# Performance work log

Hardware: AMD Instinct MI355X
Metric: run time of the kernel (lower is better)

Reference implementation:

```python
import jax, jax.numpy as jnp
import numpy as np

VOCAB = 50000
OOV = 100
UNITS = 512
EMB = UNITS // 2
N_SENT = 32
N_WORDS = 50
B = 64


def setup_inputs() -> dict:
    key = jax.random.key(0)
    ks = jax.random.split(key, 16)
    g = lambda k, sh, s=0.02: (jax.random.normal(k, sh, dtype=jnp.float32) * s)
    inp = {
        "embedded_target": jax.random.normal(ks[0], (B, 1, EMB), dtype=jnp.float32),
        "hidden_dec": jax.random.normal(ks[1], (B, UNITS), dtype=jnp.float32),
        "encoded_sentences": jax.random.normal(ks[2], (B, N_SENT, UNITS), dtype=jnp.float32),
        "encoded_words": jax.random.normal(ks[3], (B, N_SENT, N_WORDS, UNITS), dtype=jnp.float32),
        "numeric_input": jax.random.randint(ks[4], (B, N_SENT * N_WORDS), 0, VOCAB + OOV),
        "batch_size": B,
        # GRU params (keras reset_after=True layout: 3 gates z,r,h stacked)
        "gru_Wx": g(ks[5], (EMB, 3 * UNITS)),
        "gru_Wh": g(ks[6], (UNITS, 3 * UNITS)),
        "gru_b": jnp.zeros((2, 3 * UNITS), dtype=jnp.float32),
        # attention params
        "W_att_sent": g(ks[7], (UNITS, UNITS)),
        "W_att_word": g(ks[8], (UNITS, UNITS)),
        # output projection (input is dec_units//2 after weight_dec)
        "fc_W": g(ks[9], (UNITS // 2, VOCAB)),
        "fc_b": jnp.zeros((VOCAB,), dtype=jnp.float32),
        "weight_context": g(ks[10], (UNITS, 1)),
        "weight_hidden": g(ks[11], (UNITS, 1)),
        "weight_dec": g(ks[12], (2 * UNITS, UNITS // 2)),
        "weight_input": g(ks[13], (UNITS // 2, 1)),
    }
    return inp


def _gru_step(x, h, Wx, Wh, b):
    # keras GRU cell, reset_after=True
    xm = x @ Wx + b[0]            # [B, 3U]
    hm = h @ Wh + b[1]            # [B, 3U]
    xz, xr, xh = jnp.split(xm, 3, axis=-1)
    hz, hr, hh = jnp.split(hm, 3, axis=-1)
    z = jax.nn.sigmoid(xz + hz)
    r = jax.nn.sigmoid(xr + hr)
    hcand = jnp.tanh(xh + r * hh)
    return z * h + (1.0 - z) * hcand


def reference(embedded_target, hidden_dec, encoded_sentences, encoded_words,
              gru_Wx, gru_Wh, gru_b, W_att_sent, W_att_word, fc_W, fc_b,
              weight_context, weight_hidden, weight_dec, weight_input,
              numeric_input, batch_size):
    # ---- GRU over the (length-1) target step; return last hidden ----
    def step(h, x_t):
        h2 = _gru_step(x_t, h, gru_Wx, gru_Wh, gru_b)
        return h2, None
    dec_output, _ = jax.lax.scan(step, hidden_dec, jnp.swapaxes(embedded_target, 0, 1))

    # ---- Luong (general) attention over sentences ----
    q = dec_output @ W_att_sent                              # [B, U]
    score_s = jnp.einsum("bd,bsd->bs", q, encoded_sentences)  # [B, S]
    alpha = jax.nn.softmax(score_s, axis=-1)                  # [B, S]
    context = jnp.einsum("bs,bsd->bd", alpha, encoded_sentences)  # [B, U]

    # ---- generation distribution ----
    x = jnp.concatenate([context, dec_output], axis=-1)       # [B, 2U]
    hidden_t = jnp.tanh(x @ weight_dec)                       # [B, U/2]
    gen_distr = jax.nn.softmax(hidden_t @ fc_W + fc_b, axis=-1)
    gen_distr = jnp.pad(gen_distr, ((0, 0), (0, OOV)))        # [B, V+OOV]

    # ---- hierarchical word attention (word softmax per sentence, scaled by alpha) ----
    qw = dec_output @ W_att_word                              # [B, U]
    score_w = jnp.einsum("bd,bswd->bsw", qw, encoded_words)   # [B, S, W]
    word_attn = jax.nn.softmax(score_w, axis=-1)              # softmax over words
    beta = (alpha[:, :, None] * word_attn).reshape(batch_size, -1)  # [B, S*W]

    # ---- batched scatter-add copy distribution ----
    ext = VOCAB + OOV
    bidx = jnp.arange(batch_size)[:, None]
    copy_distr = jnp.zeros((batch_size, ext), dtype=beta.dtype).at[bidx, numeric_input].add(beta)

    # ---- generation gate ----
    res1 = context @ weight_context
    res2 = dec_output @ weight_hidden
    res3 = embedded_target.reshape(batch_size, EMB) @ weight_input
    p_gen = jax.nn.sigmoid(res1 + res2 + res3)                # [B, 1]

    return dec_output, gen_distr, copy_distr, p_gen
```

## Files before the change

kernel.cpp:

```cpp
#include <hip/hip_runtime.h>

#define VOCAB 50000
#define OOV   100
#define EXT   50100
#define UNITS 512
#define EMB   256
#define NS    32
#define NW    50
#define BATCH 64
#define NQ    8
#define BINS_PER ((EXT + NQ - 1) / NQ)

#define GKC   24
#define QKC   8
#define HKC   16
#define CTXS  4
#define NCB   ((VOCAB + 63) / 64)

using short8 = __attribute__((ext_vector_type(8))) short;
using f32x4  = __attribute__((ext_vector_type(4))) float;

__device__ __forceinline__ float sigmoidf_(float x) { return 1.f / (1.f + __expf(-x)); }

__device__ __forceinline__ unsigned short f2bf(float x) {
  union { float f; unsigned u; } c; c.f = x;
  const unsigned r = (c.u + 0x7FFFu + ((c.u >> 16) & 1u)) >> 16;
  return (unsigned short)r;
}

__global__ __launch_bounds__(256) void k_gru_part(
    const float* __restrict__ emb, const float* __restrict__ h0,
    const float* __restrict__ Wx, const float* __restrict__ Wh,
    float* __restrict__ gates)
{
  __shared__ float sv[32];
  const int kc = blockIdx.x, b = blockIdx.y, t = threadIdx.x, u0 = 2 * t;
  const int base = kc * 32;
  const bool isx = base < EMB;
  if (t < 32) sv[t] = isx ? emb[b * EMB + base + t] : h0[b * UNITS + base - EMB + t];
  __syncthreads();

  const float* W = isx ? (Wx + (size_t)base * 1536) : (Wh + (size_t)(base - EMB) * 1536);
  float azx = 0.f, azy = 0.f, arx = 0.f, ary = 0.f, ahx = 0.f, ahy = 0.f;
  for (int i = 0; i < 32; i += 4) {
    float2 wz[4], wr[4], wh[4];
#pragma unroll
    for (int j = 0; j < 4; ++j) {
      const float* row = W + (size_t)(i + j) * 1536;
      wz[j] = *(const float2*)(row + u0);
      wr[j] = *(const float2*)(row + 512 + u0);
      wh[j] = *(const float2*)(row + 1024 + u0);
    }
#pragma unroll
    for (int j = 0; j < 4; ++j) {
      const float v = sv[i + j];
      azx = fmaf(v, wz[j].x, azx); azy = fmaf(v, wz[j].y, azy);
      arx = fmaf(v, wr[j].x, arx); ary = fmaf(v, wr[j].y, ary);
      ahx = fmaf(v, wh[j].x, ahx); ahy = fmaf(v, wh[j].y, ahy);
    }
  }
  float* gb_ = gates + (size_t)b * 2048;
  atomicAdd(gb_ + u0, azx);           atomicAdd(gb_ + u0 + 1, azy);
  atomicAdd(gb_ + 512 + u0, arx);     atomicAdd(gb_ + 512 + u0 + 1, ary);
  const int ho = isx ? 1024 : 1536;
  atomicAdd(gb_ + ho + u0, ahx);      atomicAdd(gb_ + ho + u0 + 1, ahy);
}

__global__ __launch_bounds__(256) void k_gru_fin(
    const float* __restrict__ gates, const float* __restrict__ gb,
    const float* __restrict__ h0, const float* __restrict__ emb,
    const float* __restrict__ whid, const float* __restrict__ winp,
    float* __restrict__ ws_dec, float* __restrict__ out_dec,
    float* __restrict__ ws_pgen)
{
  __shared__ float sred[256];
  const int b = blockIdx.x, t = threadIdx.x, u0 = 2 * t;
  const float* g_ = gates + (size_t)b * 2048;
  const float2 az  = *(const float2*)(g_ + u0);
  const float2 ar  = *(const float2*)(g_ + 512 + u0);
  const float2 ahx = *(const float2*)(g_ + 1024 + u0);
  const float2 ahh = *(const float2*)(g_ + 1536 + u0);

  const float2 b0z = *(const float2*)(gb + u0);
  const float2 b0r = *(const float2*)(gb + 512 + u0);
  const float2 b0h = *(const float2*)(gb + 1024 + u0);
  const float2 b1z = *(const float2*)(gb + 1536 + u0);
  const float2 b1r = *(const float2*)(gb + 1536 + 512 + u0);
  const float2 b1h = *(const float2*)(gb + 1536 + 1024 + u0);
  const float2 hp  = *(const float2*)(h0 + b * UNITS + u0);

  const float z0 = sigmoidf_(az.x + b0z.x + b1z.x);
  const float z1 = sigmoidf_(az.y + b0z.y + b1z.y);
  const float r0 = sigmoidf_(ar.x + b0r.x + b1r.x);
  const float r1 = sigmoidf_(ar.y + b0r.y + b1r.y);
  const float c0 = tanhf(ahx.x + b0h.x + r0 * (ahh.x + b1h.x));
  const float c1 = tanhf(ahx.y + b0h.y + r1 * (ahh.y + b1h.y));
  const float n0 = z0 * hp.x + (1.f - z0) * c0;
  const float n1 = z1 * hp.y + (1.f - z1) * c1;
  ws_dec[b * UNITS + u0]      = n0;
  ws_dec[b * UNITS + u0 + 1]  = n1;
  out_dec[b * UNITS + u0]     = n0;
  out_dec[b * UNITS + u0 + 1] = n1;

  float p = n0 * whid[u0] + n1 * whid[u0 + 1];
  if (u0 < EMB) p += emb[b * EMB + u0] * winp[u0] + emb[b * EMB + u0 + 1] * winp[u0 + 1];
  sred[t] = p;
  __syncthreads();
  for (int off = 128; off > 0; off >>= 1) {
    if (t < off) sred[t] += sred[t + off];
    __syncthreads();
  }
  if (t == 0) atomicAdd(ws_pgen + b, sred[0]);
}

__global__ __launch_bounds__(256) void k_qq(
    const float* __restrict__ ws_dec, const float* __restrict__ Wsent,
    const float* __restrict__ Wword, float* __restrict__ qsum)
{
  __shared__ float sdec[64];
  const int kc = blockIdx.x, b = blockIdx.y, t = threadIdx.x, u0 = 2 * t;
  const int k0 = kc * 64;
  if (t < 64) sdec[t] = ws_dec[b * UNITS + k0 + t];
  __syncthreads();

  float qx = 0.f, qy = 0.f, wx = 0.f, wy = 0.f;
  for (int i = 0; i < 64; i += 4) {
    float2 a[4], c[4];
#pragma unroll
    for (int j = 0; j < 4; ++j) {
      a[j] = *(const float2*)(Wsent + (size_t)(k0 + i + j) * UNITS + u0);
      c[j] = *(const float2*)(Wword + (size_t)(k0 + i + j) * UNITS + u0);
    }
#pragma unroll
    for (int j = 0; j < 4; ++j) {
      const float d = sdec[i + j];
      qx = fmaf(d, a[j].x, qx); qy = fmaf(d, a[j].y, qy);
      wx = fmaf(d, c[j].x, wx); wy = fmaf(d, c[j].y, wy);
    }
  }
  float* o = qsum + (size_t)b * 1024;
  atomicAdd(o + u0, qx);           atomicAdd(o + u0 + 1, qy);
  atomicAdd(o + 512 + u0, wx);     atomicAdd(o + 512 + u0 + 1, wy);
}

__global__ __launch_bounds__(256) void k_attn_score(
    const float* __restrict__ qsum, const float* __restrict__ encS,
    float* __restrict__ ws_alpha)
{
  __shared__ float sq[UNITS];
  __shared__ float sscore[NS];
  const int b = blockIdx.x, t = threadIdx.x, u0 = 2 * t;
  *(float2*)(sq + u0) = *(const float2*)(qsum + (size_t)b * 1024 + u0);
  __syncthreads();

  const int wave = t >> 6, lane = t & 63;
  float qr[8];
#pragma unroll
  for (int j = 0; j < 8; ++j) qr[j] = sq[lane * 8 + j];
  for (int s = wave; s < NS; s += 4) {
    const float* base = encS + ((size_t)(b * NS + s)) * UNITS + lane * 8;
    const float4 v0 = *(const float4*)(base);
    const float4 v1 = *(const float4*)(base + 4);
    float acc = 0.f;
    acc = fmaf(v0.x, qr[0], acc); acc = fmaf(v0.y, qr[1], acc);
    acc = fmaf(v0.z, qr[2], acc); acc = fmaf(v0.w, qr[3], acc);
    acc = fmaf(v1.x, qr[4], acc); acc = fmaf(v1.y, qr[5], acc);
    acc = fmaf(v1.z, qr[6], acc); acc = fmaf(v1.w, qr[7], acc);
#pragma unroll
    for (int off = 32; off > 0; off >>= 1) acc += __shfl_down(acc, off);
    if (lane == 0) sscore[s] = acc;
  }
  __syncthreads();

  if (t < 32) {
    const float v = sscore[t];
    float m = v;
#pragma unroll
    for (int off = 16; off > 0; off >>= 1) m = fmaxf(m, __shfl_xor(m, off));
    const float e = __expf(v - m);
    float ssum = e;
#pragma unroll
    for (int off = 16; off > 0; off >>= 1) ssum += __shfl_xor(ssum, off);
    ws_alpha[b * NS + t] = e / ssum;
  }
}

__global__ __launch_bounds__(512) void k_ctx(
    const float* __restrict__ encS, const float* __restrict__ ws_alpha,
    const float* __restrict__ wctx, float* __restrict__ ctxsum,
    float* __restrict__ ws_pgen)
{
  const int sc = blockIdx.x, b = blockIdx.y, t = threadIdx.x;
  const float* al = ws_alpha + b * NS + sc * 8;
  float c = 0.f;
#pragma unroll
  for (int i = 0; i < 8; ++i)
    c = fmaf(al[i], encS[((size_t)(b * NS + sc * 8 + i)) * UNITS + t], c);
  atomicAdd(ctxsum + b * UNITS + t, c);

  float p = c * wctx[t];
#pragma unroll
  for (int off = 32; off > 0; off >>= 1) p += __shfl_down(p, off);
  if ((t & 63) == 0) atomicAdd(ws_pgen + b, p);
}

__global__ __launch_bounds__(128) void k_ht(
    const float* __restrict__ ctxsum, const float* __restrict__ ws_dec,
    const float* __restrict__ wdec, float* __restrict__ htsum)
{
  __shared__ float scat[64];
  const int kc = blockIdx.x, b = blockIdx.y, t = threadIdx.x, u0 = 2 * t;
  const int k0 = kc * 64;
  if (t < 64) {
    const int k = k0 + t;
    scat[t] = (k < UNITS) ? ctxsum[b * UNITS + k] : ws_dec[b * UNITS + k - UNITS];
  }
  __syncthreads();

  float ax = 0.f, ay = 0.f;
  for (int i = 0; i < 64; i += 8) {
    float2 w[8];
#pragma unroll
    for (int j = 0; j < 8; ++j)
      w[j] = *(const float2*)(wdec + (size_t)(k0 + i + j) * 256 + u0);
#pragma unroll
    for (int j = 0; j < 8; ++j) {
      const float v = scat[i + j];
      ax = fmaf(v, w[j].x, ax); ay = fmaf(v, w[j].y, ay);
    }
  }
  atomicAdd(htsum + b * EMB + u0, ax);
  atomicAdd(htsum + b * EMB + u0 + 1, ay);
}

__global__ __launch_bounds__(256) void k_ht_fin(
    const float* __restrict__ htsum, const float* __restrict__ ws_pgen,
    unsigned short* __restrict__ Af, float* __restrict__ out_pgen)
{
  const int rb = blockIdx.x, t = threadIdx.x, l = t & 63, kh = t >> 6;
  const int row = rb * 16 + (l & 15);
#pragma unroll
  for (int ks = kh; ks < 8; ks += 4) {
    const int k0 = ks * 32 + (l >> 4) * 8;
    const float4 h0 = *(const float4*)(htsum + row * EMB + k0);
    const float4 h1 = *(const float4*)(htsum + row * EMB + k0 + 4);
    short8 v;
    v[0] = (short)f2bf(tanhf(h0.x)); v[1] = (short)f2bf(tanhf(h0.y));
    v[2] = (short)f2bf(tanhf(h0.z)); v[3] = (short)f2bf(tanhf(h0.w));
    v[4] = (short)f2bf(tanhf(h1.x)); v[5] = (short)f2bf(tanhf(h1.y));
    v[6] = (short)f2bf(tanhf(h1.z)); v[7] = (short)f2bf(tanhf(h1.w));
    *(short8*)(Af + ((size_t)(rb * 8 + ks)) * 512 + l * 8) = v;
  }
  if (rb == 0 && t < BATCH) out_pgen[t] = sigmoidf_(ws_pgen[t]);
}

__global__ __launch_bounds__(256) void k_wprep(
    const float* __restrict__ fcW, unsigned short* __restrict__ Wf)
{
  __shared__ float tile[32][64];
  const int ks = blockIdx.x, cb = blockIdx.y, t = threadIdx.x;
  const int k = t >> 3, c0 = (t & 7) * 8;
  const int gk = ks * 32 + k;
  const int gc = cb * 64 + c0;
  if (cb < NCB - 1) {
    const float4 v0 = *(const float4*)(fcW + (size_t)gk * VOCAB + gc);
    const float4 v1 = *(const float4*)(fcW + (size_t)gk * VOCAB + gc + 4);
    tile[k][c0 + 0] = v0.x; tile[k][c0 + 1] = v0.y;
    tile[k][c0 + 2] = v0.z; tile[k][c0 + 3] = v0.w;
    tile[k][c0 + 4] = v1.x; tile[k][c0 + 5] = v1.y;
    tile[k][c0 + 6] = v1.z; tile[k][c0 + 7] = v1.w;
  } else {
#pragma unroll
    for (int j = 0; j < 8; ++j) {
      const int c = gc + j;
      tile[k][c0 + j] = (c < VOCAB) ? fcW[(size_t)gk * VOCAB + c] : 0.f;
    }
  }
  __syncthreads();

  const int f = t >> 6, l = t & 63;
  const int kk = (l >> 4) * 8, cc = f * 16 + (l & 15);
  short8 v;
#pragma unroll
  for (int j = 0; j < 8; ++j) v[j] = (short)f2bf(tile[kk + j][cc]);
  *(short8*)(Wf + ((size_t)((cb * 8 + ks) * 4 + f)) * 512 + l * 8) = v;
}

__global__ __launch_bounds__(256, 2) void k_fc(
    const unsigned short* __restrict__ Af, const unsigned short* __restrict__ Wf,
    const float* __restrict__ fcb, float* __restrict__ out_gen,
    float* __restrict__ ws_rowsum)
{
  const int cb = blockIdx.x;
  const int t = threadIdx.x, rb = t >> 6, l = t & 63;

  short8 a[8];
#pragma unroll
  for (int ks = 0; ks < 8; ++ks)
    a[ks] = *(const short8*)(Af + ((size_t)(rb * 8 + ks)) * 512 + l * 8);

  f32x4 acc0 = {0.f, 0.f, 0.f, 0.f};
  f32x4 acc1 = {0.f, 0.f, 0.f, 0.f};
  f32x4 acc2 = {0.f, 0.f, 0.f, 0.f};
  f32x4 acc3 = {0.f, 0.f, 0.f, 0.f};

  const unsigned short* wb = Wf + (size_t)cb * 32 * 512 + l * 8;
#pragma unroll 2
  for (int ks = 0; ks < 8; ++ks) {
    const short8 b0 = *(const short8*)(wb + (size_t)(ks * 4 + 0) * 512);
    const short8 b1 = *(const short8*)(wb + (size_t)(ks * 4 + 1) * 512);
    const short8 b2 = *(const short8*)(wb + (size_t)(ks * 4 + 2) * 512);
    const short8 b3 = *(const short8*)(wb + (size_t)(ks * 4 + 3) * 512);
    acc0 = __builtin_amdgcn_mfma_f32_16x16x32_bf16(a[ks], b0, acc0, 0, 0, 0);
    acc1 = __builtin_amdgcn_mfma_f32_16x16x32_bf16(a[ks], b1, acc1, 0, 0, 0);
    acc2 = __builtin_amdgcn_mfma_f32_16x16x32_bf16(a[ks], b2, acc2, 0, 0, 0);
    acc3 = __builtin_amdgcn_mfma_f32_16x16x32_bf16(a[ks], b3, acc3, 0, 0, 0);
  }

  const int colbase = cb * 64 + (l & 15);
  const int rowbase = rb * 16 + (l >> 4) * 4;
#pragma unroll
  for (int p = 0; p < 4; ++p) {
    float rs = 0.f;
    const float av[4] = {acc0[p], acc1[p], acc2[p], acc3[p]};
#pragma unroll
    for (int f = 0; f < 4; ++f) {
      const int col = colbase + f * 16;
      if (col < VOCAB) {
        const float e = __expf(av[f] + fcb[col]);
        out_gen[(size_t)(rowbase + p) * EXT + col] = e;
        rs += e;
      }
    }
    rs += __shfl_xor(rs, 1); rs += __shfl_xor(rs, 2);
    rs += __shfl_xor(rs, 4); rs += __shfl_xor(rs, 8);
    if ((l & 15) == 0) atomicAdd(ws_rowsum + rowbase + p, rs);
  }
}

__global__ __launch_bounds__(256) void k_word(
    const float* __restrict__ qsum, const float* __restrict__ encW,
    const float* __restrict__ ws_alpha, float* __restrict__ ws_beta)
{
  __shared__ float sqw[UNITS];
  __shared__ float sscore[64];
  const int bi = blockIdx.x;
  const int b = bi >> 5, s = bi & 31;
  const int t = threadIdx.x;
  sqw[t]       = qsum[(size_t)b * 1024 + 512 + t];
  sqw[t + 256] = qsum[(size_t)b * 1024 + 768 + t];
  __syncthreads();

  const int wave = t >> 6, lane = t & 63;
  float qr[8];
#pragma unroll
  for (int j = 0; j < 8; ++j) qr[j] = sqw[lane * 8 + j];
  const float* base = encW + ((size_t)(b * NS + s)) * NW * UNITS + lane * 8;

#pragma unroll
  for (int i = 0; i < 4; ++i) {
    const int r0 = i * 16 + wave * 4;
    if (r0 >= NW) break;
    float a0 = 0.f, a1 = 0.f, a2 = 0.f, a3 = 0.f;
    {
      const float* row = base + (size_t)r0 * UNITS;
      const float4 v0 = *(const float4*)(row);
      const float4 v1 = *(const float4*)(row + 4);
      a0 = v0.x*qr[0] + v0.y*qr[1] + v0.z*qr[2] + v0.w*qr[3]
         + v1.x*qr[4] + v1.y*qr[5] + v1.z*qr[6] + v1.w*qr[7];
    }
    if (r0 + 1 < NW) {
      const float* row = base + (size_t)(r0 + 1) * UNITS;
      const float4 v0 = *(const float4*)(row);
      const float4 v1 = *(const float4*)(row + 4);
      a1 = v0.x*qr[0] + v0.y*qr[1] + v0.z*qr[2] + v0.w*qr[3]
         + v1.x*qr[4] + v1.y*qr[5] + v1.z*qr[6] + v1.w*qr[7];
    }
    if (r0 + 2 < NW) {
      const float* row = base + (size_t)(r0 + 2) * UNITS;
      const float4 v0 = *(const float4*)(row);
      const float4 v1 = *(const float4*)(row + 4);
      a2 = v0.x*qr[0] + v0.y*qr[1] + v0.z*qr[2] + v0.w*qr[3]
         + v1.x*qr[4] + v1.y*qr[5] + v1.z*qr[6] + v1.w*qr[7];
    }
    if (r0 + 3 < NW) {
      const float* row = base + (size_t)(r0 + 3) * UNITS;
      const float4 v0 = *(const float4*)(row);
      const float4 v1 = *(const float4*)(row + 4);
      a3 = v0.x*qr[0] + v0.y*qr[1] + v0.z*qr[2] + v0.w*qr[3]
         + v1.x*qr[4] + v1.y*qr[5] + v1.z*qr[6] + v1.w*qr[7];
    }
#pragma unroll
    for (int off = 32; off > 0; off >>= 1) {
      a0 += __shfl_xor(a0, off);
      a1 += __shfl_xor(a1, off);
      a2 += __shfl_xor(a2, off);
      a3 += __shfl_xor(a3, off);
    }
    if (lane == 0) {
      sscore[r0] = a0;
      if (r0 + 1 < NW) sscore[r0 + 1] = a1;
      if (r0 + 2 < NW) sscore[r0 + 2] = a2;
      if (r0 + 3 < NW) sscore[r0 + 3] = a3;
    }
  }
  __syncthreads();

  if (t < 64) {
    const float v = (t < NW) ? sscore[t] : -1e30f;
    float m = v;
#pragma unroll
    for (int off = 32; off > 0; off >>= 1) m = fmaxf(m, __shfl_xor(m, off));
    const float e = (t < NW) ? __expf(v - m) : 0.f;
    float sum = e;
#pragma unroll
    for (int off = 32; off > 0; off >>= 1) sum += __shfl_xor(sum, off);
    if (t < NW)
      ws_beta[b * (NS * NW) + s * NW + t] = ws_alpha[b * NS + s] * e / sum;
  }
}

__global__ __launch_bounds__(256) void k_copy(
    const int* __restrict__ nidx, const float* __restrict__ ws_beta,
    float* __restrict__ out_copy)
{
  __shared__ float shist[BINS_PER];
  const int q = blockIdx.x, b = blockIdx.y, t = threadIdx.x;
  const int base = q * BINS_PER;
  const int len = min(BINS_PER, EXT - base);

  for (int j = t; j < BINS_PER; j += 256) shist[j] = 0.f;
  __syncthreads();

  for (int e = t; e < NS * NW; e += 256) {
    const int rel = nidx[b * (NS * NW) + e] - base;
    if (rel >= 0 && rel < len) atomicAdd(shist + rel, ws_beta[b * (NS * NW) + e]);
  }
  __syncthreads();

  for (int j = t; j < len; j += 256)
    out_copy[(size_t)b * EXT + base + j] = shist[j];
}

__global__ __launch_bounds__(256) void k_final(
    const float* __restrict__ ws_rowsum, float* __restrict__ out_gen)
{
  const int i = blockIdx.x * 256 + threadIdx.x;
  if (i >= BATCH * EXT) return;
  const int b = i / EXT, c = i - b * EXT;
  float g = 0.f;
  if (c < VOCAB) g = out_gen[i] / ws_rowsum[b];
  out_gen[i] = g;
}

extern "C" void kernel_launch(void* const* d_in, const int* in_sizes, int n_in,
                              void* d_out, int out_size, void* d_ws, size_t ws_size,
                              hipStream_t stream)
{
  const float* emb   = (const float*)d_in[0];
  const float* h0    = (const float*)d_in[1];
  const float* encS  = (const float*)d_in[2];
  const float* encW  = (const float*)d_in[3];
  const int*   nidx  = (const int*)d_in[4];
  const float* Wx    = (const float*)d_in[6];
  const float* Wh    = (const float*)d_in[7];
  const float* gb    = (const float*)d_in[8];
  const float* Wsent = (const float*)d_in[9];
  const float* Wword = (const float*)d_in[10];
  const float* fcW   = (const float*)d_in[11];
  const float* fcb   = (const float*)d_in[12];
  const float* wctx  = (const float*)d_in[13];
  const float* whid  = (const float*)d_in[14];
  const float* wdec  = (const float*)d_in[15];
  const float* winp  = (const float*)d_in[16];

  float* ws = (float*)d_ws;
  float* ws_gates  = ws;
  float* ws_qsum   = ws_gates + BATCH * 2048;
  float* ws_ctxsum = ws_qsum + BATCH * 1024;
  float* ws_htsum  = ws_ctxsum + BATCH * UNITS;
  float* ws_rowsum = ws_htsum + BATCH * EMB;
  float* ws_pgen   = ws_rowsum + BATCH;
  const size_t zfloats = (size_t)BATCH * (2048 + 1024 + 512 + 256) + 2 * BATCH;
  float* ws_dec    = ws_pgen + BATCH;
  float* ws_alpha  = ws_dec + BATCH * UNITS;
  float* ws_beta   = ws_alpha + BATCH * NS;
  unsigned short* ws_af = (unsigned short*)(ws_beta + BATCH * NS * NW);
  unsigned short* ws_wf = ws_af + 16384;

  float* out      = (float*)d_out;
  float* out_dec  = out;
  float* out_gen  = out + BATCH * UNITS;
  float* out_copy = out_gen + (size_t)BATCH * EXT;
  float* out_pgen = out_copy + (size_t)BATCH * EXT;

  hipMemsetAsync(ws, 0, zfloats * sizeof(float), stream);

  k_wprep<<<dim3(8, NCB), 256, 0, stream>>>(fcW, ws_wf);
  k_gru_part<<<dim3(GKC, BATCH), 256, 0, stream>>>(emb, h0, Wx, Wh, ws_gates);
  k_gru_fin<<<BATCH, 256, 0, stream>>>(ws_gates, gb, h0, emb, whid, winp,
                                       ws_dec, out_dec, ws_pgen);
  k_qq<<<dim3(QKC, BATCH), 256, 0, stream>>>(ws_dec, Wsent, Wword, ws_qsum);
  k_attn_score<<<BATCH, 256, 0, stream>>>(ws_qsum, encS, ws_alpha);
  k_ctx<<<dim3(CTXS, BATCH), 512, 0, stream>>>(encS, ws_alpha, wctx,
                                               ws_ctxsum, ws_pgen);
  k_ht<<<dim3(HKC, BATCH), 128, 0, stream>>>(ws_ctxsum, ws_dec, wdec, ws_htsum);
  k_ht_fin<<<4, 256, 0, stream>>>(ws_htsum, ws_pgen, ws_af, out_pgen);
  k_fc<<<NCB, 256, 0, stream>>>(ws_af, ws_wf, fcb, out_gen, ws_rowsum);
  k_word<<<BATCH * NS, 256, 0, stream>>>(ws_qsum, encW, ws_alpha, ws_beta);
  k_copy<<<dim3(NQ, BATCH), 256, 0, stream>>>(nidx, ws_beta, out_copy);
  k_final<<<(BATCH * EXT + 255) / 256, 256, 0, stream>>>(ws_rowsum, out_gen);
}
```

Measured before the change: 588.7 us.

## Fuse weight bf16 conversion into FC, merge attention and context, merge copy and normalize

Removes the separate fc_W to bf16 repack kernel. k_fc now streams fp32 weights directly into LDS with global_load_lds and converts them to bf16 in registers before the MFMAs, which avoids writing and re-reading a 25 MB bf16 copy. It also merges attention scoring with the context reduction (512 threads, no atomics on ctxsum), fuses the copy histogram and gen normalization into one vectorized kernel, and replaces round-to-nearest-even bf16 rounding with cheaper round-half-up. The cost is a 64 KB LDS tile per FC block, which lowers occupancy, and slightly different rounding.

```diff
diff --git a/kernel.cpp b/kernel.cpp
--- a/kernel.cpp
+++ b/kernel.cpp
@@ -14,18 +14,25 @@
 #define GKC   24
 #define QKC   8
 #define HKC   16
-#define CTXS  4
 #define NCB   ((VOCAB + 63) / 64)
+
+#define COPYB (NQ * BATCH)
+#define FINB  ((BATCH * (EXT / 4) + 255) / 256)
 
 using short8 = __attribute__((ext_vector_type(8))) short;
 using f32x4  = __attribute__((ext_vector_type(4))) float;
 
 __device__ __forceinline__ float sigmoidf_(float x) { return 1.f / (1.f + __expf(-x)); }
 
-__device__ __forceinline__ unsigned short f2bf(float x) {
+__device__ __forceinline__ unsigned short f2bf_(float x) {
   union { float f; unsigned u; } c; c.f = x;
-  const unsigned r = (c.u + 0x7FFFu + ((c.u >> 16) & 1u)) >> 16;
-  return (unsigned short)r;
+  return (unsigned short)((c.u + 0x8000u) >> 16);
+}
+
+__device__ __forceinline__ void gload_lds16(const void* g, void* l) {
+  __builtin_amdgcn_global_load_lds(
+      (const __attribute__((address_space(1))) unsigned int*)g,
+      (__attribute__((address_space(3))) unsigned int*)l, 16, 0, 0);
 }
 
 __global__ __launch_bounds__(256) void k_gru_part(
@@ -143,21 +150,24 @@
   atomicAdd(o + 512 + u0, wx);     atomicAdd(o + 512 + u0 + 1, wy);
 }
 
-__global__ __launch_bounds__(256) void k_attn_score(
+__global__ __launch_bounds__(512) void k_attn(
     const float* __restrict__ qsum, const float* __restrict__ encS,
-    float* __restrict__ ws_alpha)
+    const float* __restrict__ wctx, float* __restrict__ ws_alpha,
+    float* __restrict__ ctxsum, float* __restrict__ ws_pgen)
 {
   __shared__ float sq[UNITS];
   __shared__ float sscore[NS];
-  const int b = blockIdx.x, t = threadIdx.x, u0 = 2 * t;
-  *(float2*)(sq + u0) = *(const float2*)(qsum + (size_t)b * 1024 + u0);
+  __shared__ float salpha[NS];
+  __shared__ float sred[512];
+  const int b = blockIdx.x, t = threadIdx.x;
+  sq[t] = qsum[(size_t)b * 1024 + t];
   __syncthreads();
 
   const int wave = t >> 6, lane = t & 63;
   float qr[8];
 #pragma unroll
   for (int j = 0; j < 8; ++j) qr[j] = sq[lane * 8 + j];
-  for (int s = wave; s < NS; s += 4) {
+  for (int s = wave; s < NS; s += 8) {
     const float* base = encS + ((size_t)(b * NS + s)) * UNITS + lane * 8;
     const float4 v0 = *(const float4*)(base);
     const float4 v1 = *(const float4*)(base + 4);
@@ -181,27 +191,26 @@
     float ssum = e;
 #pragma unroll
     for (int off = 16; off > 0; off >>= 1) ssum += __shfl_xor(ssum, off);
-    ws_alpha[b * NS + t] = e / ssum;
-  }
-}
-
-__global__ __launch_bounds__(512) void k_ctx(
-    const float* __restrict__ encS, const float* __restrict__ ws_alpha,
-    const float* __restrict__ wctx, float* __restrict__ ctxsum,
-    float* __restrict__ ws_pgen)
-{
-  const int sc = blockIdx.x, b = blockIdx.y, t = threadIdx.x;
-  const float* al = ws_alpha + b * NS + sc * 8;
+    const float a = e / ssum;
+    salpha[t] = a;
+    ws_alpha[b * NS + t] = a;
+  }
+  __syncthreads();
+
   float c = 0.f;
-#pragma unroll
-  for (int i = 0; i < 8; ++i)
-    c = fmaf(al[i], encS[((size_t)(b * NS + sc * 8 + i)) * UNITS + t], c);
-  atomicAdd(ctxsum + b * UNITS + t, c);
+#pragma unroll 4
+  for (int s = 0; s < NS; ++s)
+    c = fmaf(salpha[s], encS[((size_t)(b * NS + s)) * UNITS + t], c);
+  ctxsum[b * UNITS + t] = c;
 
   float p = c * wctx[t];
-#pragma unroll
-  for (int off = 32; off > 0; off >>= 1) p += __shfl_down(p, off);
-  if ((t & 63) == 0) atomicAdd(ws_pgen + b, p);
+  sred[t] = p;
+  __syncthreads();
+  for (int off = 256; off > 0; off >>= 1) {
+    if (t < off) sred[t] += sred[t + off];
+    __syncthreads();
+  }
+  if (t == 0) atomicAdd(ws_pgen + b, sred[0]);
 }
 
 __global__ __launch_bounds__(128) void k_ht(
@@ -245,72 +254,63 @@
     const float4 h0 = *(const float4*)(htsum + row * EMB + k0);
     const float4 h1 = *(const float4*)(htsum + row * EMB + k0 + 4);
     short8 v;
-    v[0] = (short)f2bf(tanhf(h0.x)); v[1] = (short)f2bf(tanhf(h0.y));
-    v[2] = (short)f2bf(tanhf(h0.z)); v[3] = (short)f2bf(tanhf(h0.w));
-    v[4] = (short)f2bf(tanhf(h1.x)); v[5] = (short)f2bf(tanhf(h1.y));
-    v[6] = (short)f2bf(tanhf(h1.z)); v[7] = (short)f2bf(tanhf(h1.w));
+    v[0] = (short)f2bf_(tanhf(h0.x)); v[1] = (short)f2bf_(tanhf(h0.y));
+    v[2] = (short)f2bf_(tanhf(h0.z)); v[3] = (short)f2bf_(tanhf(h0.w));
+    v[4] = (short)f2bf_(tanhf(h1.x)); v[5] = (short)f2bf_(tanhf(h1.y));
+    v[6] = (short)f2bf_(tanhf(h1.z)); v[7] = (short)f2bf_(tanhf(h1.w));
     *(short8*)(Af + ((size_t)(rb * 8 + ks)) * 512 + l * 8) = v;
   }
   if (rb == 0 && t < BATCH) out_pgen[t] = sigmoidf_(ws_pgen[t]);
 }
 
-__global__ __launch_bounds__(256) void k_wprep(
-    const float* __restrict__ fcW, unsigned short* __restrict__ Wf)
-{
-  __shared__ float tile[32][64];
-  const int ks = blockIdx.x, cb = blockIdx.y, t = threadIdx.x;
-  const int k = t >> 3, c0 = (t & 7) * 8;
-  const int gk = ks * 32 + k;
-  const int gc = cb * 64 + c0;
-  if (cb < NCB - 1) {
-    const float4 v0 = *(const float4*)(fcW + (size_t)gk * VOCAB + gc);
-    const float4 v1 = *(const float4*)(fcW + (size_t)gk * VOCAB + gc + 4);
-    tile[k][c0 + 0] = v0.x; tile[k][c0 + 1] = v0.y;
-    tile[k][c0 + 2] = v0.z; tile[k][c0 + 3] = v0.w;
-    tile[k][c0 + 4] = v1.x; tile[k][c0 + 5] = v1.y;
-    tile[k][c0 + 6] = v1.z; tile[k][c0 + 7] = v1.w;
-  } else {
-#pragma unroll
-    for (int j = 0; j < 8; ++j) {
-      const int c = gc + j;
-      tile[k][c0 + j] = (c < VOCAB) ? fcW[(size_t)gk * VOCAB + c] : 0.f;
-    }
-  }
-  __syncthreads();
-
-  const int f = t >> 6, l = t & 63;
-  const int kk = (l >> 4) * 8, cc = f * 16 + (l & 15);
-  short8 v;
-#pragma unroll
-  for (int j = 0; j < 8; ++j) v[j] = (short)f2bf(tile[kk + j][cc]);
-  *(short8*)(Wf + ((size_t)((cb * 8 + ks) * 4 + f)) * 512 + l * 8) = v;
-}
-
 __global__ __launch_bounds__(256, 2) void k_fc(
-    const unsigned short* __restrict__ Af, const unsigned short* __restrict__ Wf,
+    const unsigned short* __restrict__ Af, const float* __restrict__ fcW,
     const float* __restrict__ fcb, float* __restrict__ out_gen,
     float* __restrict__ ws_rowsum)
 {
+  __shared__ float swt[256 * 64];
   const int cb = blockIdx.x;
   const int t = threadIdx.x, rb = t >> 6, l = t & 63;
 
+  {
+    const int c4 = l & 15;
+    const int gc = cb * 64 + c4 * 4;
+    const bool oob = (gc >= VOCAB);
+    const int kr = rb * 64 + (l >> 4);
+#pragma unroll
+    for (int q = 0; q < 16; ++q) {
+      const float* src = oob ? (fcW + c4 * 4)
+                             : (fcW + (size_t)(kr + q * 4) * VOCAB + gc);
+      gload_lds16(src, swt + rb * 4096 + q * 256);
+    }
+  }
+
   short8 a[8];
 #pragma unroll
   for (int ks = 0; ks < 8; ++ks)
     a[ks] = *(const short8*)(Af + ((size_t)(rb * 8 + ks)) * 512 + l * 8);
+
+  __syncthreads();
 
   f32x4 acc0 = {0.f, 0.f, 0.f, 0.f};
   f32x4 acc1 = {0.f, 0.f, 0.f, 0.f};
   f32x4 acc2 = {0.f, 0.f, 0.f, 0.f};
   f32x4 acc3 = {0.f, 0.f, 0.f, 0.f};
 
-  const unsigned short* wb = Wf + (size_t)cb * 32 * 512 + l * 8;
-#pragma unroll 2
+  const int cr = l & 15;
+  const int kb = (l >> 4) * 8;
+#pragma unroll
   for (int ks = 0; ks < 8; ++ks) {
-    const short8 b0 = *(const short8*)(wb + (size_t)(ks * 4 + 0) * 512);
-    const short8 b1 = *(const short8*)(wb + (size_t)(ks * 4 + 1) * 512);
-    const short8 b2 = *(const short8*)(wb + (size_t)(ks * 4 + 2) * 512);
-    const short8 b3 = *(const short8*)(wb + (size_t)(ks * 4 + 3) * 512);
+    const float* kbase = swt + (size_t)(ks * 32 + kb) * 64 + cr;
+    short8 b0, b1, b2, b3;
+#pragma unroll
+    for (int j = 0; j < 8; ++j) {
+      const float* rowp = kbase + j * 64;
+      b0[j] = (short)f2bf_(rowp[0]);
+      b1[j] = (short)f2bf_(rowp[16]);
+      b2[j] = (short)f2bf_(rowp[32]);
+      b3[j] = (short)f2bf_(rowp[48]);
+    }
     acc0 = __builtin_amdgcn_mfma_f32_16x16x32_bf16(a[ks], b0, acc0, 0, 0, 0);
     acc1 = __builtin_amdgcn_mfma_f32_16x16x32_bf16(a[ks], b1, acc1, 0, 0, 0);
     acc2 = __builtin_amdgcn_mfma_f32_16x16x32_bf16(a[ks], b2, acc2, 0, 0, 0);
@@ -420,37 +420,43 @@
   }
 }
 
-__global__ __launch_bounds__(256) void k_copy(
+__global__ __launch_bounds__(256) void k_tail(
     const int* __restrict__ nidx, const float* __restrict__ ws_beta,
-    float* __restrict__ out_copy)
+    const float* __restrict__ ws_rowsum, float* __restrict__ out_copy,
+    float* __restrict__ out_gen)
 {
   __shared__ float shist[BINS_PER];
-  const int q = blockIdx.x, b = blockIdx.y, t = threadIdx.x;
-  const int base = q * BINS_PER;
-  const int len = min(BINS_PER, EXT - base);
-
-  for (int j = t; j < BINS_PER; j += 256) shist[j] = 0.f;
-  __syncthreads();
-
-  for (int e = t; e < NS * NW; e += 256) {
-    const int rel = nidx[b * (NS * NW) + e] - base;
-    if (rel >= 0 && rel < len) atomicAdd(shist + rel, ws_beta[b * (NS * NW) + e]);
-  }
-  __syncthreads();
-
-  for (int j = t; j < len; j += 256)
-    out_copy[(size_t)b * EXT + base + j] = shist[j];
-}
-
-__global__ __launch_bounds__(256) void k_final(
-    const float* __restrict__ ws_rowsum, float* __restrict__ out_gen)
-{
-  const int i = blockIdx.x * 256 + threadIdx.x;
-  if (i >= BATCH * EXT) return;
-  const int b = i / EXT, c = i - b * EXT;
-  float g = 0.f;
-  if (c < VOCAB) g = out_gen[i] / ws_rowsum[b];
-  out_gen[i] = g;
+  const int bid = blockIdx.x, t = threadIdx.x;
+  if (bid < COPYB) {
+    const int q = bid & (NQ - 1), b = bid >> 3;
+    const int base = q * BINS_PER;
+    const int len = min(BINS_PER, EXT - base);
+
+    for (int j = t; j < BINS_PER; j += 256) shist[j] = 0.f;
+    __syncthreads();
+
+    for (int e = t; e < NS * NW; e += 256) {
+      const int rel = nidx[b * (NS * NW) + e] - base;
+      if (rel >= 0 && rel < len) atomicAdd(shist + rel, ws_beta[b * (NS * NW) + e]);
+    }
+    __syncthreads();
+
+    for (int j = t; j < len; j += 256)
+      out_copy[(size_t)b * EXT + base + j] = shist[j];
+  } else {
+    const int i4 = (bid - COPYB) * 256 + t;
+    if (i4 < BATCH * (EXT / 4)) {
+      const int b = i4 / (EXT / 4);
+      const int c4 = (i4 - b * (EXT / 4)) * 4;
+      float4 v = make_float4(0.f, 0.f, 0.f, 0.f);
+      if (c4 < VOCAB) {
+        v = *(const float4*)(out_gen + (size_t)b * EXT + c4);
+        const float inv = 1.f / ws_rowsum[b];
+        v.x *= inv; v.y *= inv; v.z *= inv; v.w *= inv;
+      }
+      *(float4*)(out_gen + (size_t)b * EXT + c4) = v;
+    }
+  }
 }
 
 extern "C" void kernel_launch(void* const* d_in, const int* in_sizes, int n_in,
@@ -486,7 +492,6 @@
   float* ws_alpha  = ws_dec + BATCH * UNITS;
   float* ws_beta   = ws_alpha + BATCH * NS;
   unsigned short* ws_af = (unsigned short*)(ws_beta + BATCH * NS * NW);
-  unsigned short* ws_wf = ws_af + 16384;
 
   float* out      = (float*)d_out;
   float* out_dec  = out;
@@ -496,18 +501,16 @@
 
   hipMemsetAsync(ws, 0, zfloats * sizeof(float), stream);
 
-  k_wprep<<<dim3(8, NCB), 256, 0, stream>>>(fcW, ws_wf);
   k_gru_part<<<dim3(GKC, BATCH), 256, 0, stream>>>(emb, h0, Wx, Wh, ws_gates);
   k_gru_fin<<<BATCH, 256, 0, stream>>>(ws_gates, gb, h0, emb, whid, winp,
                                        ws_dec, out_dec, ws_pgen);
   k_qq<<<dim3(QKC, BATCH), 256, 0, stream>>>(ws_dec, Wsent, Wword, ws_qsum);
-  k_attn_score<<<BATCH, 256, 0, stream>>>(ws_qsum, encS, ws_alpha);
-  k_ctx<<<dim3(CTXS, BATCH), 512, 0, stream>>>(encS, ws_alpha, wctx,
-                                               ws_ctxsum, ws_pgen);
+  k_attn<<<BATCH, 512, 0, stream>>>(ws_qsum, encS, wctx, ws_alpha,
+                                    ws_ctxsum, ws_pgen);
   k_ht<<<dim3(HKC, BATCH), 128, 0, stream>>>(ws_ctxsum, ws_dec, wdec, ws_htsum);
   k_ht_fin<<<4, 256, 0, stream>>>(ws_htsum, ws_pgen, ws_af, out_pgen);
-  k_fc<<<NCB, 256, 0, stream>>>(ws_af, ws_wf, fcb, out_gen, ws_rowsum);
+  k_fc<<<NCB, 256, 0, stream>>>(ws_af, fcW, fcb, out_gen, ws_rowsum);
   k_word<<<BATCH * NS, 256, 0, stream>>>(ws_qsum, encW, ws_alpha, ws_beta);
-  k_copy<<<dim3(NQ, BATCH), 256, 0, stream>>>(nidx, ws_beta, out_copy);
-  k_final<<<(BATCH * EXT + 255) / 256, 256, 0, stream>>>(ws_rowsum, out_gen);
-}
+  k_tail<<<COPYB + FINB, 256, 0, stream>>>(nidx, ws_beta, ws_rowsum,
+                                           out_copy, out_gen);
+}
```

After: 505.0 us. 1.17x faster.
